# Kernel tuning notes

Measured on AMD Instinct MI355X. Metric: run time of the kernel, lower is better.

## Reference

```python
import jax, jax.numpy as jnp
import numpy as np
from jax import lax

GROUP = 4  # rt_group_size, reflection=False


def build_weights(W):
    """Symmetrize per GConv3d.get_weight (mid layer, no reflection, no Hermitian).
    W: (O, 1, I, G, kY, kX, kT) -> (O*G, I*G, kY, kX, kT).
    Each group copy k is the previous copy rotated 90 deg in the (kY, kX) plane
    followed by a cyclic shift (+1) along the input-group axis.
    """
    base = W[:, 0]  # (O, I, G, kY, kX, kT)
    ws = [base]
    for _ in range(1, GROUP):
        r = jnp.rot90(ws[-1], k=1, axes=(-3, -2))
        ws.append(jnp.roll(r, shift=1, axis=2))  # cat([last, :-1]) on group axis
    w = jnp.stack(ws, axis=1)  # (O, G, I, G, kY, kX, kT)
    O, _, I, _, kY, kX, kT = w.shape
    return w.reshape(O * GROUP, I * GROUP, kY, kX, kT)


def setup_inputs() -> dict:
    key = jax.random.key(0)
    k1, k2, k3 = jax.random.split(key, 3)
    in_ch, out_ch, k, kT = 16, 16, 3, 3
    x = jax.random.normal(k1, (4, in_ch * GROUP, 32, 64, 64), dtype=jnp.float32)
    # kaiming-ish scale: fan_in = in_ch * GROUP * k * k * kT
    scale = 1.0 / np.sqrt(in_ch * GROUP * k * k * kT)
    W = jax.random.normal(k2, (out_ch, 1, in_ch, GROUP, k, k, kT), dtype=jnp.float32) * scale
    B = jax.random.normal(k3, (1, out_ch, 1, 1, 1), dtype=jnp.float32) * scale
    return {"x": x, "W": W, "B": B}


def reference(x, W, B):
    w = build_weights(W)  # (O*G, I*G, kY, kX, kT)
    y = lax.conv_general_dilated(
        x, w, window_strides=(1, 1, 1), padding='VALID',
        dimension_numbers=('NCDHW', 'OIDHW', 'NCDHW'))
    bias = jnp.repeat(B, GROUP, axis=1)  # repeat_interleave along channel dim
    return y + bias
```

## Files before the change

### kernel.cpp

```cpp
#include <hip/hip_runtime.h>
#include <hip/hip_bf16.h>


typedef __attribute__((ext_vector_type(8))) short bf16x8;
typedef __attribute__((ext_vector_type(4))) float f32x4;

__device__ __forceinline__ void gl_lds16(const void* g, void* l) {
    __builtin_amdgcn_global_load_lds(
        (const __attribute__((address_space(1))) unsigned int*)g,
        (__attribute__((address_space(3))) unsigned int*)l, 16, 0, 0);
}

#define WAITV(n) asm volatile("s_waitcnt vmcnt(" #n ")" ::: "memory")

__global__ __launch_bounds__(256) void build_wT(const float* __restrict__ W,
                                                __hip_bfloat16* __restrict__ wT) {
    int idx = blockIdx.x * 256 + threadIdx.x;
    if (idx >= 27 * 64 * 64) return;
    int ic = idx & 63;
    int oc = (idx >> 6) & 63;
    int tap = idx >> 12;
    int kt = tap % 3, kx = (tap / 3) % 3, ky = tap / 9;
    int o = oc >> 2, kc = oc & 3, i = ic >> 2, gs = ic & 3;
    int sy = ky, sx = kx;
    for (int t = 0; t < kc; ++t) {
        int ny = sx, nx = 2 - sy;
        sy = ny; sx = nx;
        gs = (gs + 3) & 3;
    }
    wT[idx] = __float2bfloat16(W[((o * 16 + i) * 4 + gs) * 27 + sy * 9 + sx * 3 + kt]);
}

__device__ __forceinline__ unsigned int pack2(float a, float b) {
    union { __hip_bfloat162 h2; unsigned int u; } c;
    c.h2 = __hip_bfloat162{__float2bfloat16(a), __float2bfloat16(b)};
    return c.u;
}

__global__ __launch_bounds__(256) void transpose_x(const float* __restrict__ x,
                                                   __hip_bfloat16* __restrict__ xT) {
    __shared__ unsigned int ls[64 * 37];
    int bid = blockIdx.x;
    int hq = bid & 7, d = (bid >> 3) & 31, nb = bid >> 8;
    int tid = threadIdx.x;
    int w4 = tid & 15;
    int kp = tid >> 4;

    float4 a[3][2], b[3][2];
#define LOADROW(s, hh) do {                                                          \
    const float* s0_ = x + ((((size_t)nb * 64 + 2 * kp) * 32 + d) * 64 + (hh)) * 64 + w4 * 4;        \
    const float* s1_ = x + ((((size_t)nb * 64 + 2 * (16 + kp)) * 32 + d) * 64 + (hh)) * 64 + w4 * 4; \
    a[s][0] = *(const float4*)s0_; b[s][0] = *(const float4*)(s0_ + 131072);         \
    a[s][1] = *(const float4*)s1_; b[s][1] = *(const float4*)(s1_ + 131072);         \
} while (0)

    LOADROW(0, hq * 8 + 0);
    LOADROW(1, hq * 8 + 1);
#pragma unroll
    for (int hi = 0; hi < 8; ++hi) {
        const int sc = hi % 3, sn = (hi + 2) % 3;
        asm volatile("s_waitcnt lgkmcnt(0)" ::: "memory");
        __builtin_amdgcn_s_barrier();
        if (hi < 6) LOADROW(sn, hq * 8 + hi + 2);
#pragma unroll
        for (int r = 0; r < 2; ++r) {
            int p = r * 16 + kp;
            ls[(w4 * 4 + 0) * 37 + p] = pack2(a[sc][r].x, b[sc][r].x);
            ls[(w4 * 4 + 1) * 37 + p] = pack2(a[sc][r].y, b[sc][r].y);
            ls[(w4 * 4 + 2) * 37 + p] = pack2(a[sc][r].z, b[sc][r].z);
            ls[(w4 * 4 + 3) * 37 + p] = pack2(a[sc][r].w, b[sc][r].w);
        }
        asm volatile("s_waitcnt lgkmcnt(0)" ::: "memory");
        __builtin_amdgcn_s_barrier();
        __hip_bfloat16* obase = xT + (((size_t)nb * 32 + d) * 64 + (hq * 8 + hi)) * 4096;
#pragma unroll
        for (int c = tid; c < 512; c += 256) {
            int ww = c >> 3, icc = c & 7;
            const unsigned int* q = ls + ww * 37 + icc * 4;
            uint4 v;
            v.x = q[0]; v.y = q[1]; v.z = q[2]; v.w = q[3];
            *(uint4*)(obase + ww * 64 + icc * 8) = v;
        }
    }
#undef LOADROW
}

__global__ __launch_bounds__(256, 2) void conv_mfma(const __hip_bfloat16* __restrict__ xT,
                                                    const __hip_bfloat16* __restrict__ wT,
                                                    const float* __restrict__ Bp,
                                                    float* __restrict__ out) {
    __shared__ __align__(16) short sB[6 * 4096 + 128];
    __shared__ __align__(16) short sA[3 * 4096];

    int orig = blockIdx.x;
    int bid = (orig & 7) * 240 + (orig >> 3);
    int ht = bid % 16;
    int d  = (bid / 16) % 30;
    int nb = bid / 480;
    int h0 = ht * 4;

    int tid = threadIdx.x;
    int w = tid >> 6;
    int lane = tid & 63;
    int quad = lane >> 4, col = lane & 15;

    f32x4 acc[4][4];
#pragma unroll
    for (int mt = 0; mt < 4; ++mt)
#pragma unroll
        for (int nt = 0; nt < 4; ++nt) acc[mt][nt] = (f32x4)(0.0f);

    int srcl = ((lane >> 3) << 6) + (((lane & 7) ^ (lane >> 3)) << 3);

    const __hip_bfloat16* xb = xT + (size_t)nb * 8388608 + (size_t)d * 262144;

#pragma unroll
    for (int i = 0; i < 12; ++i) {
        int p = w + i * 4;
        int hh = h0 + (p >> 3);
        if (hh > 63) hh = 63;
        gl_lds16(xb + hh * 4096 + (p & 7) * 512 + srcl, (char*)sB + p * 1024);
    }
#pragma unroll
    for (int a = 0; a < 2; ++a)
#pragma unroll
        for (int i = 0; i < 2; ++i)
            gl_lds16(wT + a * 4096 + (w * 2 + i) * 512 + srcl,
                     (char*)sA + a * 8192 + (w * 2 + i) * 1024);
    WAITV(2);
    __builtin_amdgcn_s_barrier();
    __builtin_amdgcn_sched_barrier(0);

#pragma unroll
    for (int g = 0; g < 27; ++g) {
        const int ky = g / 9, t = g % 9;
        const int kt = t % 3, kx = t / 3;
        const int slot = g % 3;

        if (g > 0) {
            if (g == 26) { WAITV(0); }
            else         { WAITV(2); }
            __builtin_amdgcn_s_barrier();
            __builtin_amdgcn_sched_barrier(0);
        }

        if (t == 0 && ky > 0) {
            const __hip_bfloat16* xcur = xb + (size_t)ky * 262144;
#pragma unroll
            for (int i = 0; i < 12; ++i) {
                int p = w + i * 4;
                int hh = h0 + (p >> 3);
                if (hh > 63) hh = 63;
                gl_lds16(xcur + hh * 4096 + (p & 7) * 512 + srcl, (char*)sB + p * 1024);
            }
        }
        if (g + 2 <= 26) {
#pragma unroll
            for (int i = 0; i < 2; ++i)
                gl_lds16(wT + (g + 2) * 4096 + (w * 2 + i) * 512 + srcl,
                         (char*)sA + ((g + 2) % 3) * 8192 + (w * 2 + i) * 1024);
        }
        if (t == 0 && ky > 0) {
            WAITV(2);
            __builtin_amdgcn_s_barrier();
            __builtin_amdgcn_sched_barrier(0);
        }

        const short* aBase = sA + slot * 4096;
        int wc = col + kt;
        const short* pb = sB + ((w + kx) * 64 + wc) * 64;
        int bswz = (quad * 8) ^ ((wc & 7) << 3);
#pragma unroll
        for (int ich = 0; ich < 2; ++ich) {
            bf16x8 af[4], bfr[4];
#pragma unroll
            for (int mt = 0; mt < 4; ++mt)
                af[mt] = *(const bf16x8*)(aBase + col * 64 + mt * 1024
                                          + (((ich * 4 + quad) ^ (col & 7)) << 3));
#pragma unroll
            for (int nt = 0; nt < 4; ++nt)
                bfr[nt] = *(const bf16x8*)(pb + ((ich * 32) ^ bswz) + nt * 1024);

            __builtin_amdgcn_s_setprio(1);
#pragma unroll
            for (int mt = 0; mt < 4; ++mt)
#pragma unroll
                for (int nt = 0; nt < 4; ++nt)
                    acc[mt][nt] = __builtin_amdgcn_mfma_f32_16x16x32_bf16(
                        af[mt], bfr[nt], acc[mt][nt], 0, 0, 0);
            __builtin_amdgcn_s_setprio(0);
        }
    }

    int hrow = h0 + w;
    if (hrow < 62) {
#pragma unroll
        for (int mt = 0; mt < 4; ++mt) {
            float bias = Bp[mt * 4 + quad];
#pragma unroll
            for (int nt = 0; nt < 4; ++nt) {
                int wp = nt * 16 + col;
                if (wp < 62) {
#pragma unroll
                    for (int r = 0; r < 4; ++r) {
                        int oc = mt * 16 + quad * 4 + r;
                        out[(((size_t)nb * 64 + oc) * 30 + d) * 3844 + hrow * 62 + wp]
                            = acc[mt][nt][r] + bias;
                    }
                }
            }
        }
    }
}

extern "C" void kernel_launch(void* const* d_in, const int* in_sizes, int n_in,
                              void* d_out, int out_size, void* d_ws, size_t ws_size,
                              hipStream_t stream) {
    const float* x = (const float*)d_in[0];
    const float* W = (const float*)d_in[1];
    const float* Bp = (const float*)d_in[2];
    float* out = (float*)d_out;

    char* ws = (char*)d_ws;
    __hip_bfloat16* wT = (__hip_bfloat16*)ws;
    __hip_bfloat16* xT = (__hip_bfloat16*)(ws + 262144);

    build_wT<<<(27 * 64 * 64 + 255) / 256, 256, 0, stream>>>(W, wT);
    transpose_x<<<4 * 32 * 8, 256, 0, stream>>>(x, xT);
    conv_mfma<<<4 * 30 * 16, 256, 0, stream>>>(xT, wT, Bp, out);
}
```

Measured before the change: 327.4 us.

## Double-buffer LDS fragment reads in registers to overlap with MFMA

Restructures the conv main loop so the A and B fragments for the next tap are read from LDS into a second register buffer while the MFMAs for the current tap execute. The barrier and wait schedule is reworked to match. Each step now waits for all outstanding loads (vmcnt 0) instead of leaving two in flight, and the third weight slot is prefetched at g==0. The extra fragment buffers roughly double VGPR usage, which may pressure occupancy at launch bounds of 2 blocks per CU, and the stricter waits may expose more global-load latency.

```diff
diff --git a/kernel.cpp b/kernel.cpp
--- a/kernel.cpp
+++ b/kernel.cpp
@@ -127,24 +127,42 @@
         for (int i = 0; i < 2; ++i)
             gl_lds16(wT + a * 4096 + (w * 2 + i) * 512 + srcl,
                      (char*)sA + a * 8192 + (w * 2 + i) * 1024);
-    WAITV(2);
+    WAITV(0);
     __builtin_amdgcn_s_barrier();
     __builtin_amdgcn_sched_barrier(0);
 
+    bf16x8 fa[2][4][2], fb[2][4][2];
+
+#define READ_FRAGS(q, p) do {                                                   \
+    const int kt_ = ((q) % 9) % 3, kx_ = ((q) % 9) / 3;                         \
+    const short* aB_ = sA + ((q) % 3) * 4096;                                   \
+    const int wc_ = col + kt_;                                                  \
+    const short* pb_ = sB + ((w + kx_) * 64 + wc_) * 64;                        \
+    const int bs_ = (quad * 8) ^ ((wc_ & 7) << 3);                              \
+    _Pragma("unroll") for (int ich_ = 0; ich_ < 2; ++ich_) {                    \
+        _Pragma("unroll") for (int mt_ = 0; mt_ < 4; ++mt_)                     \
+            fa[p][mt_][ich_] = *(const bf16x8*)(aB_ + col * 64 + mt_ * 1024     \
+                                + (((ich_ * 4 + quad) ^ (col & 7)) << 3));      \
+        _Pragma("unroll") for (int nt_ = 0; nt_ < 4; ++nt_)                     \
+            fb[p][nt_][ich_] = *(const bf16x8*)(pb_ + ((ich_ * 32) ^ bs_)       \
+                                + nt_ * 1024);                                  \
+    }                                                                           \
+} while (0)
+
 #pragma unroll
     for (int g = 0; g < 27; ++g) {
         const int ky = g / 9, t = g % 9;
-        const int kt = t % 3, kx = t / 3;
-        const int slot = g % 3;
-
-        if (g > 0) {
-            if (g == 26) { WAITV(0); }
-            else         { WAITV(2); }
+        const int cp = g & 1, np = cp ^ 1;
+
+        if (g == 0) {
+#pragma unroll
+            for (int i = 0; i < 2; ++i)
+                gl_lds16(wT + 2 * 4096 + (w * 2 + i) * 512 + srcl,
+                         (char*)sA + 2 * 8192 + (w * 2 + i) * 1024);
+        } else if (t == 0) {
+            WAITV(0);
             __builtin_amdgcn_s_barrier();
             __builtin_amdgcn_sched_barrier(0);
-        }
-
-        if (t == 0 && ky > 0) {
             const __hip_bfloat16* xcur = xb + (size_t)ky * 262144;
 #pragma unroll
             for (int i = 0; i < 12; ++i) {
@@ -153,44 +171,43 @@
                 if (hh > 63) hh = 63;
                 gl_lds16(xcur + hh * 4096 + (p & 7) * 512 + srcl, (char*)sB + p * 1024);
             }
-        }
-        if (g + 2 <= 26) {
 #pragma unroll
             for (int i = 0; i < 2; ++i)
                 gl_lds16(wT + (g + 2) * 4096 + (w * 2 + i) * 512 + srcl,
                          (char*)sA + ((g + 2) % 3) * 8192 + (w * 2 + i) * 1024);
-        }
-        if (t == 0 && ky > 0) {
             WAITV(2);
             __builtin_amdgcn_s_barrier();
             __builtin_amdgcn_sched_barrier(0);
-        }
-
-        const short* aBase = sA + slot * 4096;
-        int wc = col + kt;
-        const short* pb = sB + ((w + kx) * 64 + wc) * 64;
-        int bswz = (quad * 8) ^ ((wc & 7) << 3);
-#pragma unroll
-        for (int ich = 0; ich < 2; ++ich) {
-            bf16x8 af[4], bfr[4];
-#pragma unroll
-            for (int mt = 0; mt < 4; ++mt)
-                af[mt] = *(const bf16x8*)(aBase + col * 64 + mt * 1024
-                                          + (((ich * 4 + quad) ^ (col & 7)) << 3));
-#pragma unroll
-            for (int nt = 0; nt < 4; ++nt)
-                bfr[nt] = *(const bf16x8*)(pb + ((ich * 32) ^ bswz) + nt * 1024);
-
-            __builtin_amdgcn_s_setprio(1);
+        } else if (g < 26) {
+            WAITV(0);
+            __builtin_amdgcn_s_barrier();
+            __builtin_amdgcn_sched_barrier(0);
+            if (g + 2 <= 26) {
+#pragma unroll
+                for (int i = 0; i < 2; ++i)
+                    gl_lds16(wT + (g + 2) * 4096 + (w * 2 + i) * 512 + srcl,
+                             (char*)sA + ((g + 2) % 3) * 8192 + (w * 2 + i) * 1024);
+            }
+        }
+
+        if (t == 0) READ_FRAGS(g, cp);
+
+        if (g < 26 && t != 8) READ_FRAGS(g + 1, np);
+
+        __builtin_amdgcn_sched_barrier(0);
+
+        __builtin_amdgcn_s_setprio(1);
+#pragma unroll
+        for (int ich = 0; ich < 2; ++ich)
 #pragma unroll
             for (int mt = 0; mt < 4; ++mt)
 #pragma unroll
                 for (int nt = 0; nt < 4; ++nt)
                     acc[mt][nt] = __builtin_amdgcn_mfma_f32_16x16x32_bf16(
-                        af[mt], bfr[nt], acc[mt][nt], 0, 0, 0);
-            __builtin_amdgcn_s_setprio(0);
-        }
-    }
+                        fa[cp][mt][ich], fb[cp][nt][ich], acc[mt][nt], 0, 0, 0);
+        __builtin_amdgcn_s_setprio(0);
+    }
+#undef READ_FRAGS
 
     int hrow = h0 + w;
     if (hrow < 62) {
```

Measured after the change: 326.7 us. Within noise of the previous version (-0.2%).
